# Kernel tuning notes

Hardware: AMD Instinct MI355X
Metric: run time of the kernel (lower is better)

Reference implementation:

```python
import jax, jax.numpy as jnp
import numpy as np

V, C, COUT, DEG = 50000, 128, 256, 16
E = V * DEG


def setup_inputs() -> dict:
    key = jax.random.key(0)
    k1, k2, k3, k4 = jax.random.split(key, 4)
    data = jax.random.normal(k1, (V, C), dtype=jnp.float32)
    # Every vertex gets exactly DEG neighbors -> sorted segment ids.
    edge_src = jnp.repeat(jnp.arange(V, dtype=jnp.int32), DEG)
    edge_dst = jax.random.randint(k2, (E,), 0, V, dtype=jnp.int32)
    # Row-normalized neighbor weights (sum over each vertex's edges == 1).
    raw_w = jax.random.uniform(k3, (E,), dtype=jnp.float32) + 0.1
    row_sum = jax.ops.segment_sum(raw_w, edge_src, num_segments=V)
    edge_w = raw_w / row_sum[edge_src]
    kernel = jax.random.normal(k4, (2 * C, COUT), dtype=jnp.float32) * (1.0 / np.sqrt(2 * C))
    bias = jnp.zeros((COUT,), dtype=jnp.float32)
    return {"data": data, "edge_src": edge_src, "edge_dst": edge_dst,
            "edge_w": edge_w, "kernel": kernel, "bias": bias}


def reference(data, edge_src, edge_dst, edge_w, kernel, bias):
    # Gather per-edge endpoint features: x = data[i], y = data[j].
    x = data[edge_src]                       # [E, C]
    y = data[edge_dst]                       # [E, C]
    # Edge function h(x, y) = Linear([x, y - x]) (1x1 Conv1D, no activation).
    feat = jnp.concatenate([x, y - x], axis=-1)          # [E, 2C]
    edge_out = feat @ kernel + bias                       # [E, COUT]
    # reduction='weighted': out[i] = sum_j w_ij * h(x_i, x_j).
    out = jax.ops.segment_sum(edge_w[:, None] * edge_out, edge_src,
                              num_segments=data.shape[0])  # [V, COUT]
    return out
```

## Files before the change

### kernel.cpp

```cpp
#include <hip/hip_runtime.h>
#include <hip/hip_bf16.h>
#include <cstdint>

#define V_N    50000
#define C_N    128
#define COUT_N 256
#define DEG_N  16
#define K2_N   256

typedef short bf16x8 __attribute__((ext_vector_type(8)));
typedef float f32x4  __attribute__((ext_vector_type(4)));

__device__ __forceinline__ unsigned short f2bf(float f) {
    union { float f; unsigned u; } a; a.f = f;
    unsigned r = a.u + 0x7fffu + ((a.u >> 16) & 1u);
    return (unsigned short)(r >> 16);
}
__device__ __forceinline__ float bflo(unsigned p) {
    union { unsigned u; float f; } a; a.u = p << 16; return a.f;
}
__device__ __forceinline__ float bfhi(unsigned p) {
    union { unsigned u; float f; } a; a.u = p & 0xffff0000u; return a.f;
}

__global__ void prep_bt_kernel(const float* __restrict__ kern,
                               unsigned short* __restrict__ bt) {
    const int k = blockIdx.x;
    const int n = threadIdx.x;
    const int idx = (((n >> 4) * 8 + (k >> 5)) * 4 + ((k >> 3) & 3)) * 128
                  + (n & 15) * 8 + (k & 7);
    bt[idx] = f2bf(kern[k * COUT_N + n]);
}

__global__ __launch_bounds__(256)
void prep_data_kernel(const float* __restrict__ data,
                      unsigned short* __restrict__ db) {
    const int i = blockIdx.x * 256 + threadIdx.x;
    const float4 f0 = *reinterpret_cast<const float4*>(data + (size_t)i * 8);
    const float4 f1 = *reinterpret_cast<const float4*>(data + (size_t)i * 8 + 4);
    union { unsigned short h[8]; uint4 q; } o;
    o.h[0] = f2bf(f0.x); o.h[1] = f2bf(f0.y); o.h[2] = f2bf(f0.z); o.h[3] = f2bf(f0.w);
    o.h[4] = f2bf(f1.x); o.h[5] = f2bf(f1.y); o.h[6] = f2bf(f1.z); o.h[7] = f2bf(f1.w);
    *reinterpret_cast<uint4*>(db + (size_t)i * 8) = o.q;
}

__global__ __launch_bounds__(512, 4)
void dgc_fused_kernel(const unsigned short* __restrict__ db,
                      const int* __restrict__ edge_dst,
                      const float* __restrict__ edge_w,
                      const unsigned short* __restrict__ btg,
                      const float* __restrict__ bias,
                      float* __restrict__ out) {
    __shared__ __align__(16) char Asm[64 * 512];

    const int tid  = threadIdx.x;
    const int lane = tid & 63;
    const int wid  = __builtin_amdgcn_readfirstlane(tid >> 6);
    const int m0   = blockIdx.x * 64;
    const int g    = lane >> 4;
    const int c    = lane & 15;

    #pragma unroll
    for (int q = 0; q < 2; ++q) {
        const int row = wid * 8 + q * 4 + g;
        const int vq  = m0 + row;
        float s[8];
        #pragma unroll
        for (int i = 0; i < 8; ++i) s[i] = 0.f;
        float Wsum = 0.f;
        uint4 xr = make_uint4(0u, 0u, 0u, 0u);
        if (vq < V_N) {
            xr = *reinterpret_cast<const uint4*>(db + (size_t)vq * C_N + c * 8);
            const int eb = vq * DEG_N;
            #pragma unroll
            for (int k = 0; k < DEG_N; ++k) {
                const int   j  = edge_dst[eb + k];
                const float wk = edge_w[eb + k];
                const uint4 r  = *reinterpret_cast<const uint4*>(
                    db + (size_t)j * C_N + c * 8);
                s[0] = fmaf(wk, bflo(r.x), s[0]);
                s[1] = fmaf(wk, bfhi(r.x), s[1]);
                s[2] = fmaf(wk, bflo(r.y), s[2]);
                s[3] = fmaf(wk, bfhi(r.y), s[3]);
                s[4] = fmaf(wk, bflo(r.z), s[4]);
                s[5] = fmaf(wk, bfhi(r.z), s[5]);
                s[6] = fmaf(wk, bflo(r.w), s[6]);
                s[7] = fmaf(wk, bfhi(r.w), s[7]);
                Wsum += wk;
            }
        }
        float u[8], v[8];
        u[0] = Wsum * bflo(xr.x); u[1] = Wsum * bfhi(xr.x);
        u[2] = Wsum * bflo(xr.y); u[3] = Wsum * bfhi(xr.y);
        u[4] = Wsum * bflo(xr.z); u[5] = Wsum * bfhi(xr.z);
        u[6] = Wsum * bflo(xr.w); u[7] = Wsum * bfhi(xr.w);
        #pragma unroll
        for (int i = 0; i < 8; ++i) v[i] = s[i] - u[i];

        uint4 up, vp;
        up.x = (unsigned)f2bf(u[0]) | ((unsigned)f2bf(u[1]) << 16);
        up.y = (unsigned)f2bf(u[2]) | ((unsigned)f2bf(u[3]) << 16);
        up.z = (unsigned)f2bf(u[4]) | ((unsigned)f2bf(u[5]) << 16);
        up.w = (unsigned)f2bf(u[6]) | ((unsigned)f2bf(u[7]) << 16);
        vp.x = (unsigned)f2bf(v[0]) | ((unsigned)f2bf(v[1]) << 16);
        vp.y = (unsigned)f2bf(v[2]) | ((unsigned)f2bf(v[3]) << 16);
        vp.z = (unsigned)f2bf(v[4]) | ((unsigned)f2bf(v[5]) << 16);
        vp.w = (unsigned)f2bf(v[6]) | ((unsigned)f2bf(v[7]) << 16);

        const int sw   = row & 7;
        char*     rowp = Asm + row * 512;
        *reinterpret_cast<uint4*>(rowp + ((c        ^ sw) * 16)) = up;
        *reinterpret_cast<uint4*>(rowp + (((16 + c) ^ sw) * 16)) = vp;
    }
    __syncthreads();

    const int wm = wid >> 2;
    const int wn = wid & 3;

    f32x4 acc[2][4];
    #pragma unroll
    for (int mf = 0; mf < 2; ++mf)
        #pragma unroll
        for (int nf = 0; nf < 4; ++nf)
            acc[mf][nf] = (f32x4){0.f, 0.f, 0.f, 0.f};

    #pragma unroll
    for (int ks = 0; ks < 8; ++ks) {
        bf16x8 a[2], b[4];
        #pragma unroll
        for (int mf = 0; mf < 2; ++mf) {
            const int r  = wm * 32 + mf * 16 + c;
            const int ck = (ks * 4 + g) ^ (r & 7);
            a[mf] = *reinterpret_cast<const bf16x8*>(Asm + r * 512 + ck * 16);
        }
        #pragma unroll
        for (int nf = 0; nf < 4; ++nf) {
            const int nb = wn * 4 + nf;
            b[nf] = *reinterpret_cast<const bf16x8*>(
                btg + (size_t)((nb * 32 + ks * 4 + g) * 16 + c) * 8);
        }
        #pragma unroll
        for (int mf = 0; mf < 2; ++mf)
            #pragma unroll
            for (int nf = 0; nf < 4; ++nf)
                acc[mf][nf] = __builtin_amdgcn_mfma_f32_16x16x32_bf16(
                    a[mf], b[nf], acc[mf][nf], 0, 0, 0);
    }

    #pragma unroll
    for (int mf = 0; mf < 2; ++mf) {
        const int row_l = wm * 32 + mf * 16 + g * 4;
        #pragma unroll
        for (int nf = 0; nf < 4; ++nf) {
            const int col = wn * 64 + nf * 16 + c;
            const float bb = bias[col];
            #pragma unroll
            for (int r = 0; r < 4; ++r) {
                const int rg = m0 + row_l + r;
                if (rg < V_N)
                    out[(size_t)rg * COUT_N + col] = acc[mf][nf][r] + bb;
            }
        }
    }
}

extern "C" void kernel_launch(void* const* d_in, const int* in_sizes, int n_in,
                              void* d_out, int out_size, void* d_ws, size_t ws_size,
                              hipStream_t stream) {
    const float* data     = (const float*)d_in[0];
    const int*   edge_dst = (const int*)d_in[2];
    const float* edge_w   = (const float*)d_in[3];
    const float* kern     = (const float*)d_in[4];
    const float* bias     = (const float*)d_in[5];
    float*       out      = (float*)d_out;

    unsigned short* bt = (unsigned short*)d_ws;
    unsigned short* db = (unsigned short*)d_ws + (size_t)K2_N * COUT_N;

    prep_bt_kernel<<<K2_N, COUT_N, 0, stream>>>(kern, bt);
    prep_data_kernel<<<(V_N * C_N / 8) / 256, 256, 0, stream>>>(data, db);

    const int nblk = (V_N + 63) / 64;
    dgc_fused_kernel<<<nblk, 512, 0, stream>>>(db, edge_dst, edge_w, bt, bias, out);
}
```

Measured before the change: 141.7 us.

## Stage neighbor gathers via async global-to-LDS loads and merge prep kernels

Neighbor feature rows are now fetched with global_load_lds directly into per-wave LDS staging buffers, in four rounds of four edges per vertex. Edge indices for the next round are prefetched in double-buffered registers, and edge weights are broadcast across lanes with shuffles. Blocks shrink to 32 vertices and 256 threads, with each wave owning a 64-column slice of the GEMM. The two prep kernels are merged into one launch. The aim is more gather bytes in flight and less launch overhead, at the cost of a full vmcnt(0) wait each round and more LDS per block.

```diff
diff --git a/kernel.cpp b/kernel.cpp
--- a/kernel.cpp
+++ b/kernel.cpp
@@ -11,6 +11,9 @@
 typedef short bf16x8 __attribute__((ext_vector_type(8)));
 typedef float f32x4  __attribute__((ext_vector_type(4)));
 
+typedef const __attribute__((address_space(1))) void* gas_ptr;
+typedef __attribute__((address_space(3))) void*       las_ptr;
+
 __device__ __forceinline__ unsigned short f2bf(float f) {
     union { float f; unsigned u; } a; a.f = f;
     unsigned r = a.u + 0x7fffu + ((a.u >> 16) & 1u);
@@ -23,99 +26,125 @@
     union { unsigned u; float f; } a; a.u = p & 0xffff0000u; return a.f;
 }
 
-__global__ void prep_bt_kernel(const float* __restrict__ kern,
-                               unsigned short* __restrict__ bt) {
-    const int k = blockIdx.x;
-    const int n = threadIdx.x;
-    const int idx = (((n >> 4) * 8 + (k >> 5)) * 4 + ((k >> 3) & 3)) * 128
-                  + (n & 15) * 8 + (k & 7);
-    bt[idx] = f2bf(kern[k * COUT_N + n]);
-}
-
 __global__ __launch_bounds__(256)
-void prep_data_kernel(const float* __restrict__ data,
-                      unsigned short* __restrict__ db) {
-    const int i = blockIdx.x * 256 + threadIdx.x;
-    const float4 f0 = *reinterpret_cast<const float4*>(data + (size_t)i * 8);
-    const float4 f1 = *reinterpret_cast<const float4*>(data + (size_t)i * 8 + 4);
-    union { unsigned short h[8]; uint4 q; } o;
-    o.h[0] = f2bf(f0.x); o.h[1] = f2bf(f0.y); o.h[2] = f2bf(f0.z); o.h[3] = f2bf(f0.w);
-    o.h[4] = f2bf(f1.x); o.h[5] = f2bf(f1.y); o.h[6] = f2bf(f1.z); o.h[7] = f2bf(f1.w);
-    *reinterpret_cast<uint4*>(db + (size_t)i * 8) = o.q;
-}
-
-__global__ __launch_bounds__(512, 4)
+void prep_kernel(const float* __restrict__ data, const float* __restrict__ kern,
+                 unsigned short* __restrict__ db, unsigned short* __restrict__ bt) {
+    const int b = blockIdx.x;
+    if (b < 3125) {
+        const int i = b * 256 + threadIdx.x;
+        const float4 f0 = *reinterpret_cast<const float4*>(data + (size_t)i * 8);
+        const float4 f1 = *reinterpret_cast<const float4*>(data + (size_t)i * 8 + 4);
+        union { unsigned short h[8]; uint4 q; } o;
+        o.h[0] = f2bf(f0.x); o.h[1] = f2bf(f0.y); o.h[2] = f2bf(f0.z); o.h[3] = f2bf(f0.w);
+        o.h[4] = f2bf(f1.x); o.h[5] = f2bf(f1.y); o.h[6] = f2bf(f1.z); o.h[7] = f2bf(f1.w);
+        *reinterpret_cast<uint4*>(db + (size_t)i * 8) = o.q;
+    } else {
+        const int k = b - 3125;
+        const int n = threadIdx.x;
+        const int idx = (((n >> 4) * 8 + (k >> 5)) * 4 + ((k >> 3) & 3)) * 128
+                      + (n & 15) * 8 + (k & 7);
+        bt[idx] = f2bf(kern[k * COUT_N + n]);
+    }
+}
+
+__global__ __launch_bounds__(256, 3)
 void dgc_fused_kernel(const unsigned short* __restrict__ db,
                       const int* __restrict__ edge_dst,
                       const float* __restrict__ edge_w,
                       const unsigned short* __restrict__ btg,
                       const float* __restrict__ bias,
                       float* __restrict__ out) {
-    __shared__ __align__(16) char Asm[64 * 512];
+    __shared__ __align__(16) char Asm[32 * 512];
+    __shared__ __align__(16) char Stage[4][8192];
 
     const int tid  = threadIdx.x;
     const int lane = tid & 63;
     const int wid  = __builtin_amdgcn_readfirstlane(tid >> 6);
-    const int m0   = blockIdx.x * 64;
+    const int m0   = blockIdx.x * 32;
     const int g    = lane >> 4;
     const int c    = lane & 15;
-
-    #pragma unroll
-    for (int q = 0; q < 2; ++q) {
-        const int row = wid * 8 + q * 4 + g;
-        const int vq  = m0 + row;
-        float s[8];
-        #pragma unroll
-        for (int i = 0; i < 8; ++i) s[i] = 0.f;
-        float Wsum = 0.f;
-        uint4 xr = make_uint4(0u, 0u, 0u, 0u);
-        if (vq < V_N) {
-            xr = *reinterpret_cast<const uint4*>(db + (size_t)vq * C_N + c * 8);
-            const int eb = vq * DEG_N;
-            #pragma unroll
-            for (int k = 0; k < DEG_N; ++k) {
-                const int   j  = edge_dst[eb + k];
-                const float wk = edge_w[eb + k];
-                const uint4 r  = *reinterpret_cast<const uint4*>(
-                    db + (size_t)j * C_N + c * 8);
-                s[0] = fmaf(wk, bflo(r.x), s[0]);
-                s[1] = fmaf(wk, bfhi(r.x), s[1]);
-                s[2] = fmaf(wk, bflo(r.y), s[2]);
-                s[3] = fmaf(wk, bfhi(r.y), s[3]);
-                s[4] = fmaf(wk, bflo(r.z), s[4]);
-                s[5] = fmaf(wk, bfhi(r.z), s[5]);
-                s[6] = fmaf(wk, bflo(r.w), s[6]);
-                s[7] = fmaf(wk, bfhi(r.w), s[7]);
-                Wsum += wk;
+    const int vb   = m0 + wid * 8;
+
+    unsigned* stg = reinterpret_cast<unsigned*>(Stage[wid]);
+
+    const int wv = min(vb + (lane >> 3), V_N - 1);
+    const float w0r = edge_w[wv * DEG_N + (lane & 7)];
+    const float w1r = edge_w[wv * DEG_N + 8 + (lane & 7)];
+
+    float wsum = w0r + w1r;
+    wsum += __shfl_xor(wsum, 1);
+    wsum += __shfl_xor(wsum, 2);
+    wsum += __shfl_xor(wsum, 4);
+
+    unsigned xr[8];
+    #pragma unroll
+    for (int v = 0; v < 8; ++v) {
+        const int cv = min(vb + v, V_N - 1);
+        xr[v] = *reinterpret_cast<const unsigned*>(db + (size_t)cv * C_N + lane * 2);
+    }
+
+    float s[8][2];
+    #pragma unroll
+    for (int v = 0; v < 8; ++v) { s[v][0] = 0.f; s[v][1] = 0.f; }
+
+    int jbuf[2][8];
+    #pragma unroll
+    for (int i = 0; i < 8; ++i) {
+        const int cv = min(vb + i, V_N - 1);
+        jbuf[0][i] = edge_dst[cv * DEG_N + g];
+    }
+
+    #pragma unroll
+    for (int r = 0; r < 4; ++r) {
+        #pragma unroll
+        for (int i = 0; i < 8; ++i) {
+            const unsigned short* src = db + (size_t)jbuf[r & 1][i] * C_N + c * 8;
+            __builtin_amdgcn_global_load_lds((gas_ptr)(const void*)src,
+                                             (las_ptr)(void*)(Stage[wid] + i * 1024),
+                                             16, 0, 0);
+        }
+        if (r < 3) {
+            #pragma unroll
+            for (int i = 0; i < 8; ++i) {
+                const int cv = min(vb + i, V_N - 1);
+                jbuf[(r + 1) & 1][i] = edge_dst[cv * DEG_N + (r + 1) * 4 + g];
             }
         }
-        float u[8], v[8];
-        u[0] = Wsum * bflo(xr.x); u[1] = Wsum * bfhi(xr.x);
-        u[2] = Wsum * bflo(xr.y); u[3] = Wsum * bfhi(xr.y);
-        u[4] = Wsum * bflo(xr.z); u[5] = Wsum * bfhi(xr.z);
-        u[6] = Wsum * bflo(xr.w); u[7] = Wsum * bfhi(xr.w);
-        #pragma unroll
-        for (int i = 0; i < 8; ++i) v[i] = s[i] - u[i];
-
-        uint4 up, vp;
-        up.x = (unsigned)f2bf(u[0]) | ((unsigned)f2bf(u[1]) << 16);
-        up.y = (unsigned)f2bf(u[2]) | ((unsigned)f2bf(u[3]) << 16);
-        up.z = (unsigned)f2bf(u[4]) | ((unsigned)f2bf(u[5]) << 16);
-        up.w = (unsigned)f2bf(u[6]) | ((unsigned)f2bf(u[7]) << 16);
-        vp.x = (unsigned)f2bf(v[0]) | ((unsigned)f2bf(v[1]) << 16);
-        vp.y = (unsigned)f2bf(v[2]) | ((unsigned)f2bf(v[3]) << 16);
-        vp.z = (unsigned)f2bf(v[4]) | ((unsigned)f2bf(v[5]) << 16);
-        vp.w = (unsigned)f2bf(v[6]) | ((unsigned)f2bf(v[7]) << 16);
-
-        const int sw   = row & 7;
-        char*     rowp = Asm + row * 512;
-        *reinterpret_cast<uint4*>(rowp + ((c        ^ sw) * 16)) = up;
-        *reinterpret_cast<uint4*>(rowp + (((16 + c) ^ sw) * 16)) = vp;
+        asm volatile("s_waitcnt vmcnt(0)" ::: "memory");
+        __builtin_amdgcn_sched_barrier(0);
+        #pragma unroll
+        for (int v = 0; v < 8; ++v) {
+            #pragma unroll
+            for (int k = 0; k < 4; ++k) {
+                const unsigned p = stg[v * 256 + k * 64 + lane];
+                const float wk = __shfl((r & 2) ? w1r : w0r,
+                                        v * 8 + (r & 1) * 4 + k);
+                s[v][0] = fmaf(wk, bflo(p), s[v][0]);
+                s[v][1] = fmaf(wk, bfhi(p), s[v][1]);
+            }
+        }
+    }
+
+    #pragma unroll
+    for (int v = 0; v < 8; ++v) {
+        const float Ws = __shfl(wsum, v * 8);
+        const float ux = Ws * bflo(xr[v]);
+        const float uy = Ws * bfhi(xr[v]);
+        const float vx = s[v][0] - ux;
+        const float vy = s[v][1] - uy;
+        const int row = wid * 8 + v;
+        const int sw  = row & 7;
+        const int cu  = lane >> 2;
+        const int within = (lane & 3) * 4;
+        char* rowp = Asm + row * 512;
+        *reinterpret_cast<unsigned*>(rowp + ((cu        ^ sw) * 16 + within)) =
+            (unsigned)f2bf(ux) | ((unsigned)f2bf(uy) << 16);
+        *reinterpret_cast<unsigned*>(rowp + (((16 + cu) ^ sw) * 16 + within)) =
+            (unsigned)f2bf(vx) | ((unsigned)f2bf(vy) << 16);
     }
     __syncthreads();
 
-    const int wm = wid >> 2;
-    const int wn = wid & 3;
+    const int wn = wid;
 
     f32x4 acc[2][4];
     #pragma unroll
@@ -129,9 +158,9 @@
         bf16x8 a[2], b[4];
         #pragma unroll
         for (int mf = 0; mf < 2; ++mf) {
-            const int r  = wm * 32 + mf * 16 + c;
-            const int ck = (ks * 4 + g) ^ (r & 7);
-            a[mf] = *reinterpret_cast<const bf16x8*>(Asm + r * 512 + ck * 16);
+            const int rr = mf * 16 + c;
+            const int ck = (ks * 4 + g) ^ (rr & 7);
+            a[mf] = *reinterpret_cast<const bf16x8*>(Asm + rr * 512 + ck * 16);
         }
         #pragma unroll
         for (int nf = 0; nf < 4; ++nf) {
@@ -149,7 +178,7 @@
 
     #pragma unroll
     for (int mf = 0; mf < 2; ++mf) {
-        const int row_l = wm * 32 + mf * 16 + g * 4;
+        const int row_l = mf * 16 + g * 4;
         #pragma unroll
         for (int nf = 0; nf < 4; ++nf) {
             const int col = wn * 64 + nf * 16 + c;
@@ -177,9 +206,8 @@
     unsigned short* bt = (unsigned short*)d_ws;
     unsigned short* db = (unsigned short*)d_ws + (size_t)K2_N * COUT_N;
 
-    prep_bt_kernel<<<K2_N, COUT_N, 0, stream>>>(kern, bt);
-    prep_data_kernel<<<(V_N * C_N / 8) / 256, 256, 0, stream>>>(data, db);
-
-    const int nblk = (V_N + 63) / 64;
-    dgc_fused_kernel<<<nblk, 512, 0, stream>>>(db, edge_dst, edge_w, bt, bias, out);
-}
+    prep_kernel<<<3125 + 256, 256, 0, stream>>>(data, kern, db, bt);
+
+    const int nblk = (V_N + 31) / 32;
+    dgc_fused_kernel<<<nblk, 256, 0, stream>>>(db, edge_dst, edge_w, bt, bias, out);
+}
```

Result: no change. 139.4 us (-1.6%).

## Gather neighbor features in FP8, merge prep kernels, halve rows per block

Applied to the files above, without the earlier changes.

Converts the feature table to FP8 (e4m3) instead of bf16, which halves the bytes moved by the random neighbor gather. It also fuses the two preparation kernels into one launch and reads the self features directly in fp32. Edge indices and weights are now loaded as vectors, with all eight gathers issued before the accumulation. Each block handles 32 vertices instead of 64, which doubles the block count. FP8 quantization of neighbor features adds noticeable numerical error that may exceed the tolerance.

```diff
diff --git a/kernel.cpp b/kernel.cpp
--- a/kernel.cpp
+++ b/kernel.cpp
@@ -10,93 +10,113 @@
 
 typedef short bf16x8 __attribute__((ext_vector_type(8)));
 typedef float f32x4  __attribute__((ext_vector_type(4)));
+typedef float f32x2  __attribute__((ext_vector_type(2)));
 
 __device__ __forceinline__ unsigned short f2bf(float f) {
     union { float f; unsigned u; } a; a.f = f;
     unsigned r = a.u + 0x7fffu + ((a.u >> 16) & 1u);
     return (unsigned short)(r >> 16);
 }
-__device__ __forceinline__ float bflo(unsigned p) {
-    union { unsigned u; float f; } a; a.u = p << 16; return a.f;
-}
-__device__ __forceinline__ float bfhi(unsigned p) {
-    union { unsigned u; float f; } a; a.u = p & 0xffff0000u; return a.f;
-}
-
-__global__ void prep_bt_kernel(const float* __restrict__ kern,
-                               unsigned short* __restrict__ bt) {
-    const int k = blockIdx.x;
-    const int n = threadIdx.x;
-    const int idx = (((n >> 4) * 8 + (k >> 5)) * 4 + ((k >> 3) & 3)) * 128
-                  + (n & 15) * 8 + (k & 7);
-    bt[idx] = f2bf(kern[k * COUT_N + n]);
-}
 
 __global__ __launch_bounds__(256)
-void prep_data_kernel(const float* __restrict__ data,
-                      unsigned short* __restrict__ db) {
-    const int i = blockIdx.x * 256 + threadIdx.x;
-    const float4 f0 = *reinterpret_cast<const float4*>(data + (size_t)i * 8);
-    const float4 f1 = *reinterpret_cast<const float4*>(data + (size_t)i * 8 + 4);
-    union { unsigned short h[8]; uint4 q; } o;
-    o.h[0] = f2bf(f0.x); o.h[1] = f2bf(f0.y); o.h[2] = f2bf(f0.z); o.h[3] = f2bf(f0.w);
-    o.h[4] = f2bf(f1.x); o.h[5] = f2bf(f1.y); o.h[6] = f2bf(f1.z); o.h[7] = f2bf(f1.w);
-    *reinterpret_cast<uint4*>(db + (size_t)i * 8) = o.q;
+void prep_kernel(const float* __restrict__ data, const float* __restrict__ kern,
+                 unsigned* __restrict__ db8, unsigned short* __restrict__ bt) {
+    const int b = blockIdx.x;
+    if (b < 3125) {
+        const int i = b * 256 + threadIdx.x;
+        const float4 f0 = *reinterpret_cast<const float4*>(data + (size_t)i * 8);
+        const float4 f1 = *reinterpret_cast<const float4*>(data + (size_t)i * 8 + 4);
+        unsigned lo = 0, hi = 0;
+        lo = __builtin_amdgcn_cvt_pk_fp8_f32(f0.x, f0.y, lo, false);
+        lo = __builtin_amdgcn_cvt_pk_fp8_f32(f0.z, f0.w, lo, true);
+        hi = __builtin_amdgcn_cvt_pk_fp8_f32(f1.x, f1.y, hi, false);
+        hi = __builtin_amdgcn_cvt_pk_fp8_f32(f1.z, f1.w, hi, true);
+        uint2 o; o.x = lo; o.y = hi;
+        *reinterpret_cast<uint2*>(db8 + (size_t)i * 2) = o;
+    } else {
+        const int k = b - 3125;
+        const int n = threadIdx.x;
+        const int idx = (((n >> 4) * 8 + (k >> 5)) * 4 + ((k >> 3) & 3)) * 128
+                      + (n & 15) * 8 + (k & 7);
+        bt[idx] = f2bf(kern[k * COUT_N + n]);
+    }
 }
 
 __global__ __launch_bounds__(512, 4)
-void dgc_fused_kernel(const unsigned short* __restrict__ db,
+void dgc_fused_kernel(const float* __restrict__ data,
+                      const unsigned char* __restrict__ db8,
                       const int* __restrict__ edge_dst,
                       const float* __restrict__ edge_w,
                       const unsigned short* __restrict__ btg,
                       const float* __restrict__ bias,
                       float* __restrict__ out) {
-    __shared__ __align__(16) char Asm[64 * 512];
+    __shared__ __align__(16) char Asm[32 * 512];
 
     const int tid  = threadIdx.x;
     const int lane = tid & 63;
     const int wid  = __builtin_amdgcn_readfirstlane(tid >> 6);
-    const int m0   = blockIdx.x * 64;
+    const int m0   = blockIdx.x * 32;
     const int g    = lane >> 4;
     const int c    = lane & 15;
 
+    const int row = wid * 4 + g;
+    const int cv  = min(m0 + row, V_N - 1);
+
+    const uint4*  ed4 = reinterpret_cast<const uint4*>(edge_dst + (size_t)cv * DEG_N);
+    const float4* ew4 = reinterpret_cast<const float4*>(edge_w  + (size_t)cv * DEG_N);
+
+    const float4 xa = *reinterpret_cast<const float4*>(data + (size_t)cv * C_N + c * 8);
+    const float4 xb = *reinterpret_cast<const float4*>(data + (size_t)cv * C_N + c * 8 + 4);
+
+    float s[8];
     #pragma unroll
-    for (int q = 0; q < 2; ++q) {
-        const int row = wid * 8 + q * 4 + g;
-        const int vq  = m0 + row;
-        float s[8];
+    for (int i = 0; i < 8; ++i) s[i] = 0.f;
+    float Ws = 0.f;
+
+    #pragma unroll
+    for (int half = 0; half < 2; ++half) {
+        const uint4  jq0 = ed4[half * 2 + 0];
+        const uint4  jq1 = ed4[half * 2 + 1];
+        const float4 wq0 = ew4[half * 2 + 0];
+        const float4 wq1 = ew4[half * 2 + 1];
+        const unsigned jj[8] = { jq0.x, jq0.y, jq0.z, jq0.w,
+                                 jq1.x, jq1.y, jq1.z, jq1.w };
+        const float    ww[8] = { wq0.x, wq0.y, wq0.z, wq0.w,
+                                 wq1.x, wq1.y, wq1.z, wq1.w };
+
+        uint2 h[8];
         #pragma unroll
-        for (int i = 0; i < 8; ++i) s[i] = 0.f;
-        float Wsum = 0.f;
-        uint4 xr = make_uint4(0u, 0u, 0u, 0u);
-        if (vq < V_N) {
-            xr = *reinterpret_cast<const uint4*>(db + (size_t)vq * C_N + c * 8);
-            const int eb = vq * DEG_N;
-            #pragma unroll
-            for (int k = 0; k < DEG_N; ++k) {
-                const int   j  = edge_dst[eb + k];
-                const float wk = edge_w[eb + k];
-                const uint4 r  = *reinterpret_cast<const uint4*>(
-                    db + (size_t)j * C_N + c * 8);
-                s[0] = fmaf(wk, bflo(r.x), s[0]);
-                s[1] = fmaf(wk, bfhi(r.x), s[1]);
-                s[2] = fmaf(wk, bflo(r.y), s[2]);
-                s[3] = fmaf(wk, bfhi(r.y), s[3]);
-                s[4] = fmaf(wk, bflo(r.z), s[4]);
-                s[5] = fmaf(wk, bfhi(r.z), s[5]);
-                s[6] = fmaf(wk, bflo(r.w), s[6]);
-                s[7] = fmaf(wk, bfhi(r.w), s[7]);
-                Wsum += wk;
-            }
+        for (int e = 0; e < 8; ++e)
+            h[e] = *reinterpret_cast<const uint2*>(
+                db8 + (size_t)jj[e] * C_N + c * 8);
+        __builtin_amdgcn_sched_barrier(0);
+
+        #pragma unroll
+        for (int e = 0; e < 8; ++e) {
+            const f32x2 p0 = __builtin_amdgcn_cvt_pk_f32_fp8(h[e].x, false);
+            const f32x2 p1 = __builtin_amdgcn_cvt_pk_f32_fp8(h[e].x, true);
+            const f32x2 p2 = __builtin_amdgcn_cvt_pk_f32_fp8(h[e].y, false);
+            const f32x2 p3 = __builtin_amdgcn_cvt_pk_f32_fp8(h[e].y, true);
+            const float wk = ww[e];
+            s[0] = fmaf(wk, p0[0], s[0]);
+            s[1] = fmaf(wk, p0[1], s[1]);
+            s[2] = fmaf(wk, p1[0], s[2]);
+            s[3] = fmaf(wk, p1[1], s[3]);
+            s[4] = fmaf(wk, p2[0], s[4]);
+            s[5] = fmaf(wk, p2[1], s[5]);
+            s[6] = fmaf(wk, p3[0], s[6]);
+            s[7] = fmaf(wk, p3[1], s[7]);
         }
+        Ws += ((ww[0] + ww[1]) + (ww[2] + ww[3]))
+            + ((ww[4] + ww[5]) + (ww[6] + ww[7]));
+    }
+
+    {
         float u[8], v[8];
-        u[0] = Wsum * bflo(xr.x); u[1] = Wsum * bfhi(xr.x);
-        u[2] = Wsum * bflo(xr.y); u[3] = Wsum * bfhi(xr.y);
-        u[4] = Wsum * bflo(xr.z); u[5] = Wsum * bfhi(xr.z);
-        u[6] = Wsum * bflo(xr.w); u[7] = Wsum * bfhi(xr.w);
+        u[0] = Ws * xa.x; u[1] = Ws * xa.y; u[2] = Ws * xa.z; u[3] = Ws * xa.w;
+        u[4] = Ws * xb.x; u[5] = Ws * xb.y; u[6] = Ws * xb.z; u[7] = Ws * xb.w;
         #pragma unroll
         for (int i = 0; i < 8; ++i) v[i] = s[i] - u[i];
-
         uint4 up, vp;
         up.x = (unsigned)f2bf(u[0]) | ((unsigned)f2bf(u[1]) << 16);
         up.y = (unsigned)f2bf(u[2]) | ((unsigned)f2bf(u[3]) << 16);
@@ -106,9 +126,8 @@
         vp.y = (unsigned)f2bf(v[2]) | ((unsigned)f2bf(v[3]) << 16);
         vp.z = (unsigned)f2bf(v[4]) | ((unsigned)f2bf(v[5]) << 16);
         vp.w = (unsigned)f2bf(v[6]) | ((unsigned)f2bf(v[7]) << 16);
-
-        const int sw   = row & 7;
-        char*     rowp = Asm + row * 512;
+        const int sw = row & 7;
+        char* rowp = Asm + row * 512;
         *reinterpret_cast<uint4*>(rowp + ((c        ^ sw) * 16)) = up;
         *reinterpret_cast<uint4*>(rowp + (((16 + c) ^ sw) * 16)) = vp;
     }
@@ -117,21 +136,18 @@
     const int wm = wid >> 2;
     const int wn = wid & 3;
 
-    f32x4 acc[2][4];
+    f32x4 acc[4];
     #pragma unroll
-    for (int mf = 0; mf < 2; ++mf)
-        #pragma unroll
-        for (int nf = 0; nf < 4; ++nf)
-            acc[mf][nf] = (f32x4){0.f, 0.f, 0.f, 0.f};
+    for (int nf = 0; nf < 4; ++nf)
+        acc[nf] = (f32x4){0.f, 0.f, 0.f, 0.f};
 
     #pragma unroll
     for (int ks = 0; ks < 8; ++ks) {
-        bf16x8 a[2], b[4];
-        #pragma unroll
-        for (int mf = 0; mf < 2; ++mf) {
-            const int r  = wm * 32 + mf * 16 + c;
+        bf16x8 a, b[4];
+        {
+            const int r  = wm * 16 + c;
             const int ck = (ks * 4 + g) ^ (r & 7);
-            a[mf] = *reinterpret_cast<const bf16x8*>(Asm + r * 512 + ck * 16);
+            a = *reinterpret_cast<const bf16x8*>(Asm + r * 512 + ck * 16);
         }
         #pragma unroll
         for (int nf = 0; nf < 4; ++nf) {
@@ -140,16 +156,12 @@
                 btg + (size_t)((nb * 32 + ks * 4 + g) * 16 + c) * 8);
         }
         #pragma unroll
-        for (int mf = 0; mf < 2; ++mf)
-            #pragma unroll
-            for (int nf = 0; nf < 4; ++nf)
-                acc[mf][nf] = __builtin_amdgcn_mfma_f32_16x16x32_bf16(
-                    a[mf], b[nf], acc[mf][nf], 0, 0, 0);
+        for (int nf = 0; nf < 4; ++nf)
+            acc[nf] = __builtin_amdgcn_mfma_f32_16x16x32_bf16(a, b[nf], acc[nf], 0, 0, 0);
     }
 
-    #pragma unroll
-    for (int mf = 0; mf < 2; ++mf) {
-        const int row_l = wm * 32 + mf * 16 + g * 4;
+    {
+        const int row_l = wm * 16 + g * 4;
         #pragma unroll
         for (int nf = 0; nf < 4; ++nf) {
             const int col = wn * 64 + nf * 16 + c;
@@ -158,7 +170,7 @@
             for (int r = 0; r < 4; ++r) {
                 const int rg = m0 + row_l + r;
                 if (rg < V_N)
-                    out[(size_t)rg * COUT_N + col] = acc[mf][nf][r] + bb;
+                    out[(size_t)rg * COUT_N + col] = acc[nf][r] + bb;
             }
         }
     }
@@ -174,12 +186,11 @@
     const float* bias     = (const float*)d_in[5];
     float*       out      = (float*)d_out;
 
-    unsigned short* bt = (unsigned short*)d_ws;
-    unsigned short* db = (unsigned short*)d_ws + (size_t)K2_N * COUT_N;
+    unsigned short* bt  = (unsigned short*)d_ws;
+    unsigned char*  db8 = (unsigned char*)d_ws + 131072;
 
-    prep_bt_kernel<<<K2_N, COUT_N, 0, stream>>>(kern, bt);
-    prep_data_kernel<<<(V_N * C_N / 8) / 256, 256, 0, stream>>>(data, db);
+    prep_kernel<<<3125 + 256, 256, 0, stream>>>(data, kern, (unsigned*)db8, bt);
 
-    const int nblk = (V_N + 63) / 64;
-    dgc_fused_kernel<<<nblk, 512, 0, stream>>>(db, edge_dst, edge_w, bt, bias, out);
+    const int nblk = (V_N + 31) / 32;
+    dgc_fused_kernel<<<nblk, 512, 0, stream>>>(data, db8, edge_dst, edge_w, bt, bias, out);
 }
```

Measured after the change: 134.8 us. -4.8%, faster.
